# Kernel optimization log

Hardware: AMD Instinct MI355X
Metric: run time of the kernel (lower is better)

Reference implementation:

```python
import jax, jax.numpy as jnp
import numpy as np

B, L, D, H = 4, 1024, 1024, 16
HD = D // H          # head dim = 64
NUM_CASES = 8        # Sanskrit vibhakti cases
SCALE = float(np.sqrt(HD))


def setup_inputs() -> dict:
    key = jax.random.key(0)
    ks = jax.random.split(key, 13)
    s = 0.02
    return {
        "x": jax.random.normal(ks[0], (B, L, D), jnp.float32),
        "case_ids": jax.random.randint(ks[1], (B, L), 0, NUM_CASES, jnp.int32),
        "verb_mask": jax.random.randint(ks[2], (B, L), 0, 2, jnp.int32),
        "Wq": jax.random.normal(ks[3], (D, D), jnp.float32) * s,
        "bq": jnp.zeros((D,), jnp.float32),
        "Wk": jax.random.normal(ks[4], (D, D), jnp.float32) * s,
        "bk": jnp.zeros((D,), jnp.float32),
        "Wv": jax.random.normal(ks[5], (D, D), jnp.float32) * s,
        "bv": jnp.zeros((D,), jnp.float32),
        "Wo": jax.random.normal(ks[6], (D, D), jnp.float32) * s,
        "bo": jnp.zeros((D,), jnp.float32),
        "case_bias": jax.random.normal(ks[7], (H, NUM_CASES, NUM_CASES), jnp.float32) * s,
        "verb_bias": jax.random.normal(ks[8], (H,), jnp.float32) * s,
    }


def reference(x, case_ids, verb_mask, Wq, bq, Wk, bk, Wv, bv, Wo, bo, case_bias, verb_bias):
    b, l, d = x.shape

    def split_heads(t):  # [B,L,D] -> [B,H,L,HD]
        return t.reshape(b, l, H, HD).transpose(0, 2, 1, 3)

    Q = split_heads(x @ Wq + bq)
    K = split_heads(x @ Wk + bk)
    V = split_heads(x @ Wv + bv)

    scores = jnp.einsum('bhid,bhjd->bhij', Q, K) / SCALE  # [B,H,L,L]

    # Panini constraint bias: per-head case-pair bias + per-head verb-position bias
    cb = case_bias[:, case_ids[:, :, None], case_ids[:, None, :]]  # [H,B,L,L]
    cb = cb.transpose(1, 0, 2, 3)                                  # [B,H,L,L]
    vb = verb_bias[None, :, None, None] * verb_mask[:, None, None, :].astype(scores.dtype)
    scores = scores + cb + vb

    weights = jax.nn.softmax(scores, axis=-1)  # dropout is identity in eval
    out = jnp.einsum('bhij,bhjd->bhid', weights, V)       # [B,H,L,HD]
    out = out.transpose(0, 2, 1, 3).reshape(b, l, d)
    return out @ Wo + bo
```

## Files before the change

kernel.cpp:

```cpp
#include <hip/hip_runtime.h>

#define BB 4
#define LL 1024
#define DD 1024
#define HH 16
#define HDD 64

typedef __bf16 bf16x8 __attribute__((ext_vector_type(8)));
typedef float f32x4 __attribute__((ext_vector_type(4)));
typedef float f32x16 __attribute__((ext_vector_type(16)));
typedef unsigned short u16x8 __attribute__((ext_vector_type(8)));
typedef unsigned short u16x4 __attribute__((ext_vector_type(4)));
typedef unsigned int u32x4v __attribute__((ext_vector_type(4)));
typedef unsigned int u32x2 __attribute__((ext_vector_type(2)));

#define LOG2E 1.4426950408889634f

__device__ __forceinline__ unsigned short f2bf(float f) {
    unsigned int u = __builtin_bit_cast(unsigned int, f);
    u += 0x7FFFu + ((u >> 16) & 1u);
    return (unsigned short)(u >> 16);
}

__device__ __forceinline__ unsigned int cvtpk_bf16(float lo, float hi) {
    unsigned int r;
    asm("v_cvt_pk_bf16_f32 %0, %1, %2" : "=v"(r) : "v"(lo), "v"(hi));
    return r;
}

__global__ __launch_bounds__(256) void cvt_x(const float* __restrict__ x,
                                             unsigned short* __restrict__ xb) {
    const int i = (blockIdx.x * 256 + threadIdx.x) * 8;
    f32x4 a0 = *(const f32x4*)(x + i);
    f32x4 a1 = *(const f32x4*)(x + i + 4);
    u16x8 o;
#pragma unroll
    for (int j = 0; j < 4; ++j) { o[j] = f2bf(a0[j]); o[4 + j] = f2bf(a1[j]); }
    *(u16x8*)(xb + i) = o;
}

__global__ __launch_bounds__(256) void trans_w(const float* __restrict__ Wq,
                                               const float* __restrict__ Wk,
                                               const float* __restrict__ Wv,
                                               const float* __restrict__ Wo,
                                               unsigned short* __restrict__ Wqkv_t,
                                               unsigned short* __restrict__ Wo_t) {
    __shared__ unsigned short lds[64 * 72];
    const int t = threadIdx.x;
    const int mat = blockIdx.z;
    const float* W = (mat == 0) ? Wq : (mat == 1) ? Wk : (mat == 2) ? Wv : Wo;
    unsigned short* out = (mat < 3) ? (Wqkv_t + (size_t)mat * 1024 * 1024) : Wo_t;
    const int k0 = blockIdx.x * 64;
    const int n0 = blockIdx.y * 64;
#pragma unroll
    for (int p = 0; p < 4; ++p) {
        int c = t + p * 256;
        int kr = c >> 4, c4 = (c & 15) * 4;
        f32x4 v = *(const f32x4*)(W + (size_t)(k0 + kr) * 1024 + n0 + c4);
#pragma unroll
        for (int i = 0; i < 4; ++i) lds[(c4 + i) * 72 + kr] = f2bf(v[i]);
    }
    __syncthreads();
#pragma unroll
    for (int p = 0; p < 2; ++p) {
        int c = t + p * 256;
        int nr = c >> 3, koff = (c & 7) * 8;
        u16x8 vv = *(const u16x8*)&lds[nr * 72 + koff];
        *(u16x8*)(out + (size_t)(n0 + nr) * 1024 + k0 + koff) = vv;
    }
}

__global__ __launch_bounds__(256) void gemm_qkv(const unsigned short* __restrict__ Abf,
                                                const unsigned short* __restrict__ Btw,
                                                const float* __restrict__ bq,
                                                const float* __restrict__ bk,
                                                const float* __restrict__ bv,
                                                unsigned short* __restrict__ qkv) {
    __shared__ unsigned short Asm[128 * 32];
    __shared__ unsigned short Bsm[128 * 32];
    const int t = threadIdx.x;
    const int w = t >> 6, lane = t & 63;
    const int wm = w >> 1, wn = w & 1;
    const int lr = lane & 15, lk = (lane >> 4) * 8;
    const int row0 = blockIdx.x * 128;
    const int col0 = blockIdx.y * 128;
    const int r = t >> 2;
    const int cb8 = (t & 3) * 8;

    f32x4 acc[4][4];
#pragma unroll
    for (int mf = 0; mf < 4; ++mf)
#pragma unroll
        for (int nf = 0; nf < 4; ++nf)
#pragma unroll
            for (int e = 0; e < 4; ++e) acc[mf][nf][e] = 0.f;

    for (int kt = 0; kt < 32; ++kt) {
        __syncthreads();
        const int k0 = kt * 32;
#pragma unroll
        for (int p = 0; p < 2; ++p) {
            const unsigned short* sa = Abf + (size_t)(row0 + p * 64 + r) * 1024 + k0 + cb8;
            __builtin_amdgcn_global_load_lds(
                (const __attribute__((address_space(1))) unsigned int*)sa,
                (__attribute__((address_space(3))) unsigned int*)(Asm + p * 2048 + t * 8), 16, 0, 0);
            const unsigned short* sb = Btw + (size_t)(col0 + p * 64 + r) * 1024 + k0 + cb8;
            __builtin_amdgcn_global_load_lds(
                (const __attribute__((address_space(1))) unsigned int*)sb,
                (__attribute__((address_space(3))) unsigned int*)(Bsm + p * 2048 + t * 8), 16, 0, 0);
        }
        __syncthreads();
        bf16x8 af[4], bfr[4];
#pragma unroll
        for (int mf = 0; mf < 4; ++mf)
            af[mf] = *(const bf16x8*)&Asm[(wm * 64 + mf * 16 + lr) * 32 + lk];
#pragma unroll
        for (int nf = 0; nf < 4; ++nf)
            bfr[nf] = *(const bf16x8*)&Bsm[(wn * 64 + nf * 16 + lr) * 32 + lk];
#pragma unroll
        for (int mf = 0; mf < 4; ++mf)
#pragma unroll
            for (int nf = 0; nf < 4; ++nf)
                acc[mf][nf] = __builtin_amdgcn_mfma_f32_16x16x32_bf16(af[mf], bfr[nf], acc[mf][nf], 0, 0, 0);
    }

#pragma unroll
    for (int mf = 0; mf < 4; ++mf) {
        const int grow = row0 + wm * 64 + mf * 16 + (lane >> 4) * 4;
#pragma unroll
        for (int nf = 0; nf < 4; ++nf) {
            const int gcol = col0 + wn * 64 + nf * 16 + lr;
            const int mat = gcol >> 10;
            const int nc_ = gcol & 1023;
            const float bias = (mat == 0) ? bq[nc_] : (mat == 1 ? bk[nc_] : bv[nc_]);
            const float scale = (mat == 0) ? 0.125f * LOG2E : 1.0f;
            const int hh = nc_ >> 6, hd = nc_ & 63;
#pragma unroll
            for (int rr = 0; rr < 4; ++rr) {
                const int row = grow + rr;
                const int bb = row >> 10, ll = row & 1023;
                const float vout = (acc[mf][nf][rr] + bias) * scale;
                qkv[((((size_t)mat * BB + bb) * HH + hh) * LL + ll) * HDD + hd] = f2bf(vout);
            }
        }
    }
}

__global__ __launch_bounds__(256) void vtrans(const unsigned short* __restrict__ Vg,
                                              unsigned short* __restrict__ Vt) {
    __shared__ unsigned short lds[64 * 72];
    const int t = threadIdx.x;
    const int bh = blockIdx.y;
    const int j0 = blockIdx.x * 64;
    const size_t hoff = (size_t)bh * LL * HDD;
#pragma unroll
    for (int p = 0; p < 2; ++p) {
        int c = t + p * 256;
        int jr = c >> 3, doff = (c & 7) * 8;
        u16x8 v = *(const u16x8*)(Vg + hoff + (size_t)(j0 + jr) * 64 + doff);
#pragma unroll
        for (int i = 0; i < 8; ++i) lds[(doff + i) * 72 + jr] = v[i];
    }
    __syncthreads();
#pragma unroll
    for (int p = 0; p < 2; ++p) {
        int c = t + p * 256;
        int dr = c >> 3, joff = (c & 7) * 8;
        u16x8 vv = *(const u16x8*)&lds[dr * 72 + joff];
        *(u16x8*)(Vt + hoff + (size_t)dr * 1024 + j0 + joff) = vv;
    }
}

__global__ __launch_bounds__(256) void attn2(const unsigned short* __restrict__ Qg,
                                             const unsigned short* __restrict__ Kg,
                                             const unsigned short* __restrict__ Vtg,
                                             const int* __restrict__ cid,
                                             const int* __restrict__ vmask,
                                             const float* __restrict__ case_bias,
                                             const float* __restrict__ verb_bias,
                                             unsigned short* __restrict__ att) {
    __shared__ unsigned short kvbuf[2][8192];
    __shared__ float tbl[2][8][68];

    const int t = threadIdx.x;
    const int w = t >> 6;
    const int lane = t & 63;
    const int q31 = lane & 31;
    const int g = lane >> 5;

    const int f = blockIdx.x;
    const int qt = (f >> 3) & 7;
    const int bh = ((f & 7) << 3) | (f >> 6);
    const int b = bh >> 4, h = bh & 15;
    const size_t headoff = (size_t)bh * LL * HDD;
    const int q0 = qt * 128;
    const int qrow = q0 + w * 32 + q31;

    bf16x8 qf[4];
    {
        const unsigned short* qp = Qg + headoff + (size_t)qrow * HDD + g * 8;
        qf[0] = *(const bf16x8*)(qp);
        qf[1] = *(const bf16x8*)(qp + 16);
        qf[2] = *(const bf16x8*)(qp + 32);
        qf[3] = *(const bf16x8*)(qp + 48);
    }
    const int cirow = cid[b * LL + qrow] * 68;
    const float vbh = verb_bias[h] * LOG2E;

    float m_run = -1e30f, l_run = 0.f;
    f32x16 acc0, acc1;
#pragma unroll
    for (int e = 0; e < 16; ++e) { acc0[e] = 0.f; acc1[e] = 0.f; }

    const int r8 = lane >> 3, c8 = lane & 7;

#define STAGE(bufn, j0)                                                                            \
    {                                                                                              \
        _Pragma("unroll") for (int cc = 0; cc < 2; ++cc) {                                         \
            const int chunk = w + cc * 4;                                                          \
            const int row = chunk * 8 + r8;                                                        \
            const int sc8 = (c8 ^ (row & 7)) * 8;                                                  \
            const unsigned short* srck = Kg + headoff + (size_t)((j0) + row) * HDD + sc8;          \
            __builtin_amdgcn_global_load_lds(                                                      \
                (const __attribute__((address_space(1))) unsigned int*)srck,                       \
                (__attribute__((address_space(3))) unsigned int*)(&kvbuf[bufn][chunk * 512]), 16,  \
                0, 0);                                                                             \
            const unsigned short* srcv = Vtg + headoff + (size_t)row * LL + (j0) + sc8;            \
            __builtin_amdgcn_global_load_lds(                                                      \
                (const __attribute__((address_space(1))) unsigned int*)srcv,                       \
                (__attribute__((address_space(3))) unsigned int*)(&kvbuf[bufn][4096 + chunk * 512]),\
                16, 0, 0);                                                                         \
        }                                                                                          \
        const int jj = t & 63, ci0 = t >> 6;                                                       \
        const int cj = cid[b * LL + (j0) + jj];                                                    \
        const float vb = vmask[b * LL + (j0) + jj] ? vbh : 0.f;                                    \
        tbl[bufn][ci0][jj] = case_bias[h * 64 + ci0 * 8 + cj] * LOG2E + vb;                        \
        tbl[bufn][ci0 + 4][jj] = case_bias[h * 64 + (ci0 + 4) * 8 + cj] * LOG2E + vb;              \
    }

    STAGE(0, 0);
    __syncthreads();

    for (int jt = 0; jt < 16; ++jt) {
        const int buf = jt & 1;
        if (jt < 15) STAGE(buf ^ 1, (jt + 1) * 64);

        const float* tb = &tbl[buf][0][0] + cirow + 4 * g;
        f32x16 st[2];
#pragma unroll
        for (int jt2 = 0; jt2 < 2; ++jt2) {
            f32x16 s;
#pragma unroll
            for (int r = 0; r < 16; ++r) s[r] = tb[jt2 * 32 + (r & 3) + 8 * (r >> 2)];
            const int arow = jt2 * 32 + q31;
            const unsigned short* kb = &kvbuf[buf][arow * 64];
            const int swz = arow & 7;
#pragma unroll
            for (int kk = 0; kk < 4; ++kk) {
                bf16x8 af = *(const bf16x8*)&kb[((2 * kk + g) ^ swz) * 8];
                s = __builtin_amdgcn_mfma_f32_32x32x16_bf16(af, qf[kk], s, 0, 0, 0);
            }
            st[jt2] = s;
        }

        float mx[16];
#pragma unroll
        for (int r = 0; r < 16; ++r) mx[r] = fmaxf(st[0][r], st[1][r]);
#pragma unroll
        for (int d = 8; d >= 1; d >>= 1)
#pragma unroll
            for (int r = 0; r < 8; ++r)
                if (r < d) mx[r] = fmaxf(mx[r], mx[r + d]);
        float tmax = fmaxf(mx[0], __shfl_xor(mx[0], 32));

        if (!__all(tmax <= m_run + 8.f)) {
            const float mnew = fmaxf(m_run, tmax);
            const float sc = __builtin_amdgcn_exp2f(m_run - mnew);
            m_run = mnew;
            l_run *= sc;
#pragma unroll
            for (int e = 0; e < 16; ++e) { acc0[e] *= sc; acc1[e] *= sc; }
        }

        float tsum = 0.f;
#pragma unroll
        for (int jt2 = 0; jt2 < 2; ++jt2)
#pragma unroll
            for (int r = 0; r < 16; ++r) {
                const float p = __builtin_amdgcn_exp2f(st[jt2][r] - m_run);
                st[jt2][r] = p;
                tsum += p;
            }
        tsum += __shfl_xor(tsum, 32);
        l_run += tsum;

#pragma unroll
        for (int kk = 0; kk < 4; ++kk) {
            const int jt2 = kk >> 1, rb = (kk & 1) * 8;
            unsigned int a0 = cvtpk_bf16(st[jt2][rb + 0], st[jt2][rb + 1]);
            unsigned int b0 = cvtpk_bf16(st[jt2][rb + 4], st[jt2][rb + 5]);
            unsigned int a1 = cvtpk_bf16(st[jt2][rb + 2], st[jt2][rb + 3]);
            unsigned int b1 = cvtpk_bf16(st[jt2][rb + 6], st[jt2][rb + 7]);
            u32x2 r0 = __builtin_amdgcn_permlane32_swap(a0, b0, false, false);
            u32x2 r1 = __builtin_amdgcn_permlane32_swap(a1, b1, false, false);
            u32x4v pw;
            pw[0] = r0[0]; pw[1] = r1[0]; pw[2] = r0[1]; pw[3] = r1[1];
            const bf16x8 pf = __builtin_bit_cast(bf16x8, pw);
#pragma unroll
            for (int dt = 0; dt < 2; ++dt) {
                const int vrow = dt * 32 + q31;
                const bf16x8 vf =
                    *(const bf16x8*)&kvbuf[buf][4096 + vrow * 64 + (((2 * kk + g) ^ (vrow & 7)) * 8)];
                if (dt == 0)
                    acc0 = __builtin_amdgcn_mfma_f32_32x32x16_bf16(vf, pf, acc0, 0, 0, 0);
                else
                    acc1 = __builtin_amdgcn_mfma_f32_32x32x16_bf16(vf, pf, acc1, 0, 0, 0);
            }
        }
        __syncthreads();
    }

    const float inv = 1.0f / l_run;
    unsigned short* ob = &kvbuf[0][0];
    const int orow = w * 32 + q31;
    const int oswz = (orow & 7) << 3;
#pragma unroll
    for (int dt = 0; dt < 2; ++dt) {
#pragma unroll
        for (int u = 0; u < 4; ++u) {
            u16x4 v4;
#pragma unroll
            for (int v = 0; v < 4; ++v)
                v4[v] = f2bf((dt ? acc1[4 * u + v] : acc0[4 * u + v]) * inv);
            const int d0 = dt * 32 + 8 * u + 4 * g;
            *(u16x4*)&ob[orow * 64 + (d0 ^ oswz)] = v4;
        }
    }
    __syncthreads();
#pragma unroll
    for (int p = 0; p < 4; ++p) {
        const int row = p * 32 + (t >> 3);
        const int c16 = t & 7;
        u16x8 v = *(const u16x8*)&ob[row * 64 + ((c16 ^ (row & 7)) * 8)];
        *(u16x8*)(att + (size_t)(b * LL + q0 + row) * DD + h * 64 + c16 * 8) = v;
    }
#undef STAGE
}

__global__ __launch_bounds__(256) void gemm_out(const unsigned short* __restrict__ Abf,
                                                const unsigned short* __restrict__ Btw,
                                                const float* __restrict__ bo,
                                                float* __restrict__ out) {
    __shared__ unsigned short Asm[128 * 32];
    __shared__ unsigned short Bsm[128 * 32];
    const int t = threadIdx.x;
    const int w = t >> 6, lane = t & 63;
    const int wm = w >> 1, wn = w & 1;
    const int lr = lane & 15, lk = (lane >> 4) * 8;
    const int row0 = blockIdx.x * 128;
    const int col0 = blockIdx.y * 128;
    const int r = t >> 2;
    const int cb8 = (t & 3) * 8;

    f32x4 acc[4][4];
#pragma unroll
    for (int mf = 0; mf < 4; ++mf)
#pragma unroll
        for (int nf = 0; nf < 4; ++nf)
#pragma unroll
            for (int e = 0; e < 4; ++e) acc[mf][nf][e] = 0.f;

    for (int kt = 0; kt < 32; ++kt) {
        __syncthreads();
        const int k0 = kt * 32;
#pragma unroll
        for (int p = 0; p < 2; ++p) {
            const unsigned short* sa = Abf + (size_t)(row0 + p * 64 + r) * 1024 + k0 + cb8;
            __builtin_amdgcn_global_load_lds(
                (const __attribute__((address_space(1))) unsigned int*)sa,
                (__attribute__((address_space(3))) unsigned int*)(Asm + p * 2048 + t * 8), 16, 0, 0);
            const unsigned short* sb = Btw + (size_t)(col0 + p * 64 + r) * 1024 + k0 + cb8;
            __builtin_amdgcn_global_load_lds(
                (const __attribute__((address_space(1))) unsigned int*)sb,
                (__attribute__((address_space(3))) unsigned int*)(Bsm + p * 2048 + t * 8), 16, 0, 0);
        }
        __syncthreads();
        bf16x8 af[4], bfr[4];
#pragma unroll
        for (int mf = 0; mf < 4; ++mf)
            af[mf] = *(const bf16x8*)&Asm[(wm * 64 + mf * 16 + lr) * 32 + lk];
#pragma unroll
        for (int nf = 0; nf < 4; ++nf)
            bfr[nf] = *(const bf16x8*)&Bsm[(wn * 64 + nf * 16 + lr) * 32 + lk];
#pragma unroll
        for (int mf = 0; mf < 4; ++mf)
#pragma unroll
            for (int nf = 0; nf < 4; ++nf)
                acc[mf][nf] = __builtin_amdgcn_mfma_f32_16x16x32_bf16(af[mf], bfr[nf], acc[mf][nf], 0, 0, 0);
    }

#pragma unroll
    for (int mf = 0; mf < 4; ++mf) {
        const int grow = row0 + wm * 64 + mf * 16 + (lane >> 4) * 4;
#pragma unroll
        for (int nf = 0; nf < 4; ++nf) {
            const int gcol = col0 + wn * 64 + nf * 16 + lr;
            const float bias = bo[gcol];
#pragma unroll
            for (int rr = 0; rr < 4; ++rr)
                out[(size_t)(grow + rr) * 1024 + gcol] = acc[mf][nf][rr] + bias;
        }
    }
}

extern "C" void kernel_launch(void* const* d_in, const int* in_sizes, int n_in,
                              void* d_out, int out_size, void* d_ws, size_t ws_size,
                              hipStream_t stream) {
    const float* x = (const float*)d_in[0];
    const int* cid = (const int*)d_in[1];
    const int* vmask = (const int*)d_in[2];
    const float* Wq = (const float*)d_in[3];
    const float* bq = (const float*)d_in[4];
    const float* Wk = (const float*)d_in[5];
    const float* bk = (const float*)d_in[6];
    const float* Wv = (const float*)d_in[7];
    const float* bv = (const float*)d_in[8];
    const float* Wo = (const float*)d_in[9];
    const float* bo = (const float*)d_in[10];
    const float* case_bias = (const float*)d_in[11];
    const float* verb_bias = (const float*)d_in[12];
    float* out = (float*)d_out;

    char* ws = (char*)d_ws;
    unsigned short* xb     = (unsigned short*)(ws);
    unsigned short* Wqkv_t = (unsigned short*)(ws + ((size_t)8 << 20));
    unsigned short* Wo_t   = (unsigned short*)(ws + ((size_t)14 << 20));
    unsigned short* qkv    = (unsigned short*)(ws + ((size_t)16 << 20));
    unsigned short* Vt     = (unsigned short*)(ws + ((size_t)40 << 20));
    unsigned short* att    = (unsigned short*)(ws + ((size_t)48 << 20));

    const size_t MATSZ = (size_t)BB * HH * LL * HDD;

    hipLaunchKernelGGL(cvt_x, dim3(2048), dim3(256), 0, stream, x, xb);
    hipLaunchKernelGGL(trans_w, dim3(16, 16, 4), dim3(256), 0, stream, Wq, Wk, Wv, Wo, Wqkv_t, Wo_t);
    hipLaunchKernelGGL(gemm_qkv, dim3(32, 24), dim3(256), 0, stream, xb, Wqkv_t, bq, bk, bv, qkv);
    hipLaunchKernelGGL(vtrans, dim3(16, 64), dim3(256), 0, stream, qkv + 2 * MATSZ, Vt);
    hipLaunchKernelGGL(attn2, dim3(512), dim3(256), 0, stream,
                       qkv, qkv + MATSZ, Vt, cid, vmask, case_bias, verb_bias, att);
    hipLaunchKernelGGL(gemm_out, dim3(32, 8), dim3(256), 0, stream, att, Wo_t, bo, out);
}
```

Measured before the change: 108.5 us.

## Load K/V directly from global in attention, precompute bias table in separate kernel

The attention kernel no longer double-buffers K and V tiles in LDS with barriers. Each wave now reads its MFMA operands straight from global/L2 memory, and the per-iteration __syncthreads is removed. The case/verb bias table is precomputed once per (batch, head) by a new bias_prep kernel and read from global as vectors. s_setprio hints are also added around the MFMA sections. This trades LDS reuse across the 4 waves for redundant global/L2 traffic, since each wave fetches the same K/V independently, and it adds an extra kernel launch.

```diff
diff --git a/kernel.cpp b/kernel.cpp
--- a/kernel.cpp
+++ b/kernel.cpp
@@ -67,6 +67,26 @@
         int nr = c >> 3, koff = (c & 7) * 8;
         u16x8 vv = *(const u16x8*)&lds[nr * 72 + koff];
         *(u16x8*)(out + (size_t)(n0 + nr) * 1024 + k0 + koff) = vv;
+    }
+}
+
+__global__ __launch_bounds__(256) void bias_prep(const int* __restrict__ cid,
+                                                 const int* __restrict__ vmask,
+                                                 const float* __restrict__ case_bias,
+                                                 const float* __restrict__ verb_bias,
+                                                 float* __restrict__ btab) {
+    const int bh = blockIdx.x;
+    const int b = bh >> 4, h = bh & 15;
+    const float vbh = verb_bias[h] * LOG2E;
+    const int t = threadIdx.x;
+#pragma unroll
+    for (int p = 0; p < 4; ++p) {
+        const int j = t + p * 256;
+        const int cj = cid[b * LL + j];
+        const float vb = vmask[b * LL + j] ? vbh : 0.f;
+#pragma unroll
+        for (int ci = 0; ci < 8; ++ci)
+            btab[((size_t)bh * 8 + ci) * LL + j] = case_bias[h * 64 + ci * 8 + cj] * LOG2E + vb;
     }
 }
 
@@ -171,16 +191,13 @@
     }
 }
 
-__global__ __launch_bounds__(256) void attn2(const unsigned short* __restrict__ Qg,
+__global__ __launch_bounds__(256) void attn3(const unsigned short* __restrict__ Qg,
                                              const unsigned short* __restrict__ Kg,
                                              const unsigned short* __restrict__ Vtg,
                                              const int* __restrict__ cid,
-                                             const int* __restrict__ vmask,
-                                             const float* __restrict__ case_bias,
-                                             const float* __restrict__ verb_bias,
+                                             const float* __restrict__ btab,
                                              unsigned short* __restrict__ att) {
-    __shared__ unsigned short kvbuf[2][8192];
-    __shared__ float tbl[2][8][68];
+    __shared__ unsigned short ob[128 * 64];
 
     const int t = threadIdx.x;
     const int w = t >> 6;
@@ -204,62 +221,38 @@
         qf[2] = *(const bf16x8*)(qp + 32);
         qf[3] = *(const bf16x8*)(qp + 48);
     }
-    const int cirow = cid[b * LL + qrow] * 68;
-    const float vbh = verb_bias[h] * LOG2E;
+    const int ci = cid[b * LL + qrow];
+    const float* bias_base = btab + ((size_t)bh * 8 + ci) * LL + 4 * g;
 
     float m_run = -1e30f, l_run = 0.f;
     f32x16 acc0, acc1;
 #pragma unroll
     for (int e = 0; e < 16; ++e) { acc0[e] = 0.f; acc1[e] = 0.f; }
 
-    const int r8 = lane >> 3, c8 = lane & 7;
-
-#define STAGE(bufn, j0)                                                                            \
-    {                                                                                              \
-        _Pragma("unroll") for (int cc = 0; cc < 2; ++cc) {                                         \
-            const int chunk = w + cc * 4;                                                          \
-            const int row = chunk * 8 + r8;                                                        \
-            const int sc8 = (c8 ^ (row & 7)) * 8;                                                  \
-            const unsigned short* srck = Kg + headoff + (size_t)((j0) + row) * HDD + sc8;          \
-            __builtin_amdgcn_global_load_lds(                                                      \
-                (const __attribute__((address_space(1))) unsigned int*)srck,                       \
-                (__attribute__((address_space(3))) unsigned int*)(&kvbuf[bufn][chunk * 512]), 16,  \
-                0, 0);                                                                             \
-            const unsigned short* srcv = Vtg + headoff + (size_t)row * LL + (j0) + sc8;            \
-            __builtin_amdgcn_global_load_lds(                                                      \
-                (const __attribute__((address_space(1))) unsigned int*)srcv,                       \
-                (__attribute__((address_space(3))) unsigned int*)(&kvbuf[bufn][4096 + chunk * 512]),\
-                16, 0, 0);                                                                         \
-        }                                                                                          \
-        const int jj = t & 63, ci0 = t >> 6;                                                       \
-        const int cj = cid[b * LL + (j0) + jj];                                                    \
-        const float vb = vmask[b * LL + (j0) + jj] ? vbh : 0.f;                                    \
-        tbl[bufn][ci0][jj] = case_bias[h * 64 + ci0 * 8 + cj] * LOG2E + vb;                        \
-        tbl[bufn][ci0 + 4][jj] = case_bias[h * 64 + (ci0 + 4) * 8 + cj] * LOG2E + vb;              \
-    }
-
-    STAGE(0, 0);
-    __syncthreads();
+    const unsigned short* kbase = Kg + headoff + (size_t)q31 * HDD + 8 * g;
+    const unsigned short* vbase = Vtg + headoff + (size_t)q31 * LL + 8 * g;
 
     for (int jt = 0; jt < 16; ++jt) {
-        const int buf = jt & 1;
-        if (jt < 15) STAGE(buf ^ 1, (jt + 1) * 64);
-
-        const float* tb = &tbl[buf][0][0] + cirow + 4 * g;
+        const int j0 = jt * 64;
+
+        f32x4 bl[8];
+#pragma unroll
+        for (int c = 0; c < 8; ++c) bl[c] = *(const f32x4*)(bias_base + j0 + 8 * c);
+
         f32x16 st[2];
 #pragma unroll
         for (int jt2 = 0; jt2 < 2; ++jt2) {
             f32x16 s;
 #pragma unroll
-            for (int r = 0; r < 16; ++r) s[r] = tb[jt2 * 32 + (r & 3) + 8 * (r >> 2)];
-            const int arow = jt2 * 32 + q31;
-            const unsigned short* kb = &kvbuf[buf][arow * 64];
-            const int swz = arow & 7;
+            for (int r = 0; r < 16; ++r) s[r] = bl[(r >> 2) + 4 * jt2][r & 3];
+            const unsigned short* kb = kbase + (size_t)(j0 + jt2 * 32) * HDD;
+            __builtin_amdgcn_s_setprio(1);
 #pragma unroll
             for (int kk = 0; kk < 4; ++kk) {
-                bf16x8 af = *(const bf16x8*)&kb[((2 * kk + g) ^ swz) * 8];
+                bf16x8 af = *(const bf16x8*)(kb + 16 * kk);
                 s = __builtin_amdgcn_mfma_f32_32x32x16_bf16(af, qf[kk], s, 0, 0, 0);
             }
+            __builtin_amdgcn_s_setprio(0);
             st[jt2] = s;
         }
 
@@ -294,6 +287,7 @@
         tsum += __shfl_xor(tsum, 32);
         l_run += tsum;
 
+        __builtin_amdgcn_s_setprio(1);
 #pragma unroll
         for (int kk = 0; kk < 4; ++kk) {
             const int jt2 = kk >> 1, rb = (kk & 1) * 8;
@@ -308,20 +302,17 @@
             const bf16x8 pf = __builtin_bit_cast(bf16x8, pw);
 #pragma unroll
             for (int dt = 0; dt < 2; ++dt) {
-                const int vrow = dt * 32 + q31;
-                const bf16x8 vf =
-                    *(const bf16x8*)&kvbuf[buf][4096 + vrow * 64 + (((2 * kk + g) ^ (vrow & 7)) * 8)];
+                const bf16x8 vf = *(const bf16x8*)(vbase + (size_t)(dt * 32) * LL + j0 + 16 * kk);
                 if (dt == 0)
                     acc0 = __builtin_amdgcn_mfma_f32_32x32x16_bf16(vf, pf, acc0, 0, 0, 0);
                 else
                     acc1 = __builtin_amdgcn_mfma_f32_32x32x16_bf16(vf, pf, acc1, 0, 0, 0);
             }
         }
-        __syncthreads();
+        __builtin_amdgcn_s_setprio(0);
     }
 
     const float inv = 1.0f / l_run;
-    unsigned short* ob = &kvbuf[0][0];
     const int orow = w * 32 + q31;
     const int oswz = (orow & 7) << 3;
 #pragma unroll
@@ -344,7 +335,6 @@
         u16x8 v = *(const u16x8*)&ob[row * 64 + ((c16 ^ (row & 7)) * 8)];
         *(u16x8*)(att + (size_t)(b * LL + q0 + row) * DD + h * 64 + c16 * 8) = v;
     }
-#undef STAGE
 }
 
 __global__ __launch_bounds__(256) void gemm_out(const unsigned short* __restrict__ Abf,
@@ -438,14 +428,16 @@
     unsigned short* qkv    = (unsigned short*)(ws + ((size_t)16 << 20));
     unsigned short* Vt     = (unsigned short*)(ws + ((size_t)40 << 20));
     unsigned short* att    = (unsigned short*)(ws + ((size_t)48 << 20));
+    float*          btab   = (float*)(ws + ((size_t)56 << 20));
 
     const size_t MATSZ = (size_t)BB * HH * LL * HDD;
 
     hipLaunchKernelGGL(cvt_x, dim3(2048), dim3(256), 0, stream, x, xb);
     hipLaunchKernelGGL(trans_w, dim3(16, 16, 4), dim3(256), 0, stream, Wq, Wk, Wv, Wo, Wqkv_t, Wo_t);
+    hipLaunchKernelGGL(bias_prep, dim3(64), dim3(256), 0, stream, cid, vmask, case_bias, verb_bias, btab);
     hipLaunchKernelGGL(gemm_qkv, dim3(32, 24), dim3(256), 0, stream, xb, Wqkv_t, bq, bk, bv, qkv);
     hipLaunchKernelGGL(vtrans, dim3(16, 64), dim3(256), 0, stream, qkv + 2 * MATSZ, Vt);
-    hipLaunchKernelGGL(attn2, dim3(512), dim3(256), 0, stream,
-                       qkv, qkv + MATSZ, Vt, cid, vmask, case_bias, verb_bias, att);
+    hipLaunchKernelGGL(attn3, dim3(512), dim3(256), 0, stream,
+                       qkv, qkv + MATSZ, Vt, cid, btab, att);
     hipLaunchKernelGGL(gemm_out, dim3(32, 8), dim3(256), 0, stream, att, Wo_t, bo, out);
 }
```

Result: slower. 161.0 us (+48.4%).

## Precompute bias table, halve attention tile, explicit double-buffer with prefetched bias registers

Applied to the files above, without the earlier changes.

A new prep kernel builds a per-(batch, head, query-case) table of the combined case and verb bias, laid out in MFMA accumulator order. The attention kernel then loads its bias straight into registers instead of rebuilding an LDS table on every key tile. The attention kernel moves to 128 threads handling 64 query rows, with 1024 blocks and launch bounds of two blocks per unit. The key-tile loop is unrolled by two with explicit waitcnt and barrier handling, and s_setprio is raised around the MFMA sections. In exchange it adds a launch, a small extra global table, and K/V reloads across twice as many blocks.

```diff
diff --git a/kernel.cpp b/kernel.cpp
--- a/kernel.cpp
+++ b/kernel.cpp
@@ -67,6 +67,26 @@
         int nr = c >> 3, koff = (c & 7) * 8;
         u16x8 vv = *(const u16x8*)&lds[nr * 72 + koff];
         *(u16x8*)(out + (size_t)(n0 + nr) * 1024 + k0 + koff) = vv;
+    }
+}
+
+__global__ __launch_bounds__(256) void bias_prep3(const int* __restrict__ cid,
+                                                  const int* __restrict__ vmask,
+                                                  const float* __restrict__ case_bias,
+                                                  const float* __restrict__ verb_bias,
+                                                  float* __restrict__ btab3) {
+    const int bh = blockIdx.x;
+    const int b = bh >> 4, h = bh & 15;
+    const float vbh = verb_bias[h] * LOG2E;
+    for (int idx = threadIdx.x; idx < 8192; idx += 256) {
+        const int ci = idx >> 10;
+        const int g = (idx >> 9) & 1;
+        const int pos = idx & 511;
+        const int jt = pos >> 5, jt2 = (pos >> 4) & 1, r = pos & 15;
+        const int j = jt * 64 + jt2 * 32 + (r & 3) + 8 * (r >> 2) + 4 * g;
+        const int cj = cid[b * LL + j];
+        const float vb = vmask[b * LL + j] ? vbh : 0.f;
+        btab3[(size_t)bh * 8192 + idx] = case_bias[h * 64 + ci * 8 + cj] * LOG2E + vb;
     }
 }
 
@@ -171,30 +191,107 @@
     }
 }
 
-__global__ __launch_bounds__(256) void attn2(const unsigned short* __restrict__ Qg,
-                                             const unsigned short* __restrict__ Kg,
-                                             const unsigned short* __restrict__ Vtg,
-                                             const int* __restrict__ cid,
-                                             const int* __restrict__ vmask,
-                                             const float* __restrict__ case_bias,
-                                             const float* __restrict__ verb_bias,
-                                             unsigned short* __restrict__ att) {
+__device__ __forceinline__ void ctile64(const unsigned short* kvb, const f32x4 (&bb)[8],
+                                        const bf16x8 (&qf)[4], int q31, int g,
+                                        f32x16& acc0, f32x16& acc1, float& m_run, float& l_run) {
+    f32x16 st[2];
+#pragma unroll
+    for (int jt2 = 0; jt2 < 2; ++jt2) {
+        f32x16 s;
+#pragma unroll
+        for (int r = 0; r < 16; ++r) s[r] = bb[jt2 * 4 + (r >> 2)][r & 3];
+        const int arow = jt2 * 32 + q31;
+        const unsigned short* kb = &kvb[arow * 64];
+        const int swz = arow & 7;
+        __builtin_amdgcn_s_setprio(1);
+#pragma unroll
+        for (int kk = 0; kk < 4; ++kk) {
+            const bf16x8 af = *(const bf16x8*)&kb[((2 * kk + g) ^ swz) * 8];
+            s = __builtin_amdgcn_mfma_f32_32x32x16_bf16(af, qf[kk], s, 0, 0, 0);
+        }
+        __builtin_amdgcn_s_setprio(0);
+        st[jt2] = s;
+    }
+
+    float mx[16];
+#pragma unroll
+    for (int r = 0; r < 16; ++r) mx[r] = fmaxf(st[0][r], st[1][r]);
+#pragma unroll
+    for (int d = 8; d >= 1; d >>= 1)
+#pragma unroll
+        for (int r = 0; r < 8; ++r)
+            if (r < d) mx[r] = fmaxf(mx[r], mx[r + d]);
+    float tmax = fmaxf(mx[0], __shfl_xor(mx[0], 32));
+
+    if (!__all(tmax <= m_run + 8.f)) {
+        const float mnew = fmaxf(m_run, tmax);
+        const float sc = __builtin_amdgcn_exp2f(m_run - mnew);
+        m_run = mnew;
+        l_run *= sc;
+#pragma unroll
+        for (int e = 0; e < 16; ++e) { acc0[e] *= sc; acc1[e] *= sc; }
+    }
+
+    float tsum = 0.f;
+#pragma unroll
+    for (int jt2 = 0; jt2 < 2; ++jt2)
+#pragma unroll
+        for (int r = 0; r < 16; ++r) {
+            const float p = __builtin_amdgcn_exp2f(st[jt2][r] - m_run);
+            st[jt2][r] = p;
+            tsum += p;
+        }
+    tsum += __shfl_xor(tsum, 32);
+    l_run += tsum;
+
+    __builtin_amdgcn_s_setprio(1);
+#pragma unroll
+    for (int kk = 0; kk < 4; ++kk) {
+        const int jt2 = kk >> 1, rb = (kk & 1) * 8;
+        unsigned int a0 = cvtpk_bf16(st[jt2][rb + 0], st[jt2][rb + 1]);
+        unsigned int b0 = cvtpk_bf16(st[jt2][rb + 4], st[jt2][rb + 5]);
+        unsigned int a1 = cvtpk_bf16(st[jt2][rb + 2], st[jt2][rb + 3]);
+        unsigned int b1 = cvtpk_bf16(st[jt2][rb + 6], st[jt2][rb + 7]);
+        u32x2 r0 = __builtin_amdgcn_permlane32_swap(a0, b0, false, false);
+        u32x2 r1 = __builtin_amdgcn_permlane32_swap(a1, b1, false, false);
+        u32x4v pw;
+        pw[0] = r0[0]; pw[1] = r1[0]; pw[2] = r0[1]; pw[3] = r1[1];
+        const bf16x8 pf = __builtin_bit_cast(bf16x8, pw);
+#pragma unroll
+        for (int dt = 0; dt < 2; ++dt) {
+            const int vrow = dt * 32 + q31;
+            const bf16x8 vf =
+                *(const bf16x8*)&kvb[4096 + vrow * 64 + (((2 * kk + g) ^ (vrow & 7)) * 8)];
+            if (dt == 0)
+                acc0 = __builtin_amdgcn_mfma_f32_32x32x16_bf16(vf, pf, acc0, 0, 0, 0);
+            else
+                acc1 = __builtin_amdgcn_mfma_f32_32x32x16_bf16(vf, pf, acc1, 0, 0, 0);
+        }
+    }
+    __builtin_amdgcn_s_setprio(0);
+}
+
+__global__ __launch_bounds__(128, 2) void attn7(const unsigned short* __restrict__ Qg,
+                                                const unsigned short* __restrict__ Kg,
+                                                const unsigned short* __restrict__ Vtg,
+                                                const int* __restrict__ cid,
+                                                const float* __restrict__ btab3,
+                                                unsigned short* __restrict__ att) {
     __shared__ unsigned short kvbuf[2][8192];
-    __shared__ float tbl[2][8][68];
 
     const int t = threadIdx.x;
-    const int w = t >> 6;
+    const int w2 = t >> 6;
     const int lane = t & 63;
     const int q31 = lane & 31;
     const int g = lane >> 5;
 
     const int f = blockIdx.x;
-    const int qt = (f >> 3) & 7;
-    const int bh = ((f & 7) << 3) | (f >> 6);
+    const int qt = (f >> 3) & 15;
+    const int bh = ((f & 7) << 3) | (f >> 7);
     const int b = bh >> 4, h = bh & 15;
     const size_t headoff = (size_t)bh * LL * HDD;
-    const int q0 = qt * 128;
-    const int qrow = q0 + w * 32 + q31;
+    const int q0 = qt * 64;
+    const int qrow = q0 + w2 * 32 + q31;
 
     bf16x8 qf[4];
     {
@@ -204,125 +301,65 @@
         qf[2] = *(const bf16x8*)(qp + 32);
         qf[3] = *(const bf16x8*)(qp + 48);
     }
-    const int cirow = cid[b * LL + qrow] * 68;
-    const float vbh = verb_bias[h] * LOG2E;
-
-    float m_run = -1e30f, l_run = 0.f;
-    f32x16 acc0, acc1;
-#pragma unroll
-    for (int e = 0; e < 16; ++e) { acc0[e] = 0.f; acc1[e] = 0.f; }
+    const int ci = cid[b * LL + qrow];
+    const float* bbase = btab3 + ((size_t)(bh * 8 + ci) * 2 + g) * 512;
 
     const int r8 = lane >> 3, c8 = lane & 7;
 
-#define STAGE(bufn, j0)                                                                            \
+#define STAGE(bufn, j0s)                                                                           \
     {                                                                                              \
-        _Pragma("unroll") for (int cc = 0; cc < 2; ++cc) {                                         \
-            const int chunk = w + cc * 4;                                                          \
+        _Pragma("unroll") for (int cc = 0; cc < 4; ++cc) {                                         \
+            const int chunk = w2 + cc * 2;                                                         \
             const int row = chunk * 8 + r8;                                                        \
             const int sc8 = (c8 ^ (row & 7)) * 8;                                                  \
-            const unsigned short* srck = Kg + headoff + (size_t)((j0) + row) * HDD + sc8;          \
+            const unsigned short* srck = Kg + headoff + (size_t)((j0s) + row) * HDD + sc8;         \
             __builtin_amdgcn_global_load_lds(                                                      \
                 (const __attribute__((address_space(1))) unsigned int*)srck,                       \
                 (__attribute__((address_space(3))) unsigned int*)(&kvbuf[bufn][chunk * 512]), 16,  \
                 0, 0);                                                                             \
-            const unsigned short* srcv = Vtg + headoff + (size_t)row * LL + (j0) + sc8;            \
+            const unsigned short* srcv = Vtg + headoff + (size_t)row * LL + (j0s) + sc8;           \
             __builtin_amdgcn_global_load_lds(                                                      \
                 (const __attribute__((address_space(1))) unsigned int*)srcv,                       \
                 (__attribute__((address_space(3))) unsigned int*)(&kvbuf[bufn][4096 + chunk * 512]),\
                 16, 0, 0);                                                                         \
         }                                                                                          \
-        const int jj = t & 63, ci0 = t >> 6;                                                       \
-        const int cj = cid[b * LL + (j0) + jj];                                                    \
-        const float vb = vmask[b * LL + (j0) + jj] ? vbh : 0.f;                                    \
-        tbl[bufn][ci0][jj] = case_bias[h * 64 + ci0 * 8 + cj] * LOG2E + vb;                        \
-        tbl[bufn][ci0 + 4][jj] = case_bias[h * 64 + (ci0 + 4) * 8 + cj] * LOG2E + vb;              \
-    }
-
+    }
+
+    float m_run = -1e30f, l_run = 0.f;
+    f32x16 acc0, acc1;
+#pragma unroll
+    for (int e = 0; e < 16; ++e) { acc0[e] = 0.f; acc1[e] = 0.f; }
+
+    f32x4 bA[8], bB[8];
     STAGE(0, 0);
+#pragma unroll
+    for (int i = 0; i < 8; ++i) bA[i] = *(const f32x4*)(bbase + 4 * i);
+
+    for (int jt = 0; jt < 16; jt += 2) {
+        asm volatile("s_waitcnt vmcnt(0)" ::: "memory");
+        __builtin_amdgcn_s_barrier();
+        asm volatile("" ::: "memory");
+        STAGE(1, (jt + 1) * 64);
+#pragma unroll
+        for (int i = 0; i < 8; ++i) bB[i] = *(const f32x4*)(bbase + (jt + 1) * 32 + 4 * i);
+        ctile64(&kvbuf[0][0], bA, qf, q31, g, acc0, acc1, m_run, l_run);
+
+        asm volatile("s_waitcnt vmcnt(0)" ::: "memory");
+        __builtin_amdgcn_s_barrier();
+        asm volatile("" ::: "memory");
+        if (jt + 2 < 16) {
+            STAGE(0, (jt + 2) * 64);
+#pragma unroll
+            for (int i = 0; i < 8; ++i) bA[i] = *(const f32x4*)(bbase + (jt + 2) * 32 + 4 * i);
+        }
+        ctile64(&kvbuf[1][0], bB, qf, q31, g, acc0, acc1, m_run, l_run);
+    }
+#undef STAGE
+
     __syncthreads();
-
-    for (int jt = 0; jt < 16; ++jt) {
-        const int buf = jt & 1;
-        if (jt < 15) STAGE(buf ^ 1, (jt + 1) * 64);
-
-        const float* tb = &tbl[buf][0][0] + cirow + 4 * g;
-        f32x16 st[2];
-#pragma unroll
-        for (int jt2 = 0; jt2 < 2; ++jt2) {
-            f32x16 s;
-#pragma unroll
-            for (int r = 0; r < 16; ++r) s[r] = tb[jt2 * 32 + (r & 3) + 8 * (r >> 2)];
-            const int arow = jt2 * 32 + q31;
-            const unsigned short* kb = &kvbuf[buf][arow * 64];
-            const int swz = arow & 7;
-#pragma unroll
-            for (int kk = 0; kk < 4; ++kk) {
-                bf16x8 af = *(const bf16x8*)&kb[((2 * kk + g) ^ swz) * 8];
-                s = __builtin_amdgcn_mfma_f32_32x32x16_bf16(af, qf[kk], s, 0, 0, 0);
-            }
-            st[jt2] = s;
-        }
-
-        float mx[16];
-#pragma unroll
-        for (int r = 0; r < 16; ++r) mx[r] = fmaxf(st[0][r], st[1][r]);
-#pragma unroll
-        for (int d = 8; d >= 1; d >>= 1)
-#pragma unroll
-            for (int r = 0; r < 8; ++r)
-                if (r < d) mx[r] = fmaxf(mx[r], mx[r + d]);
-        float tmax = fmaxf(mx[0], __shfl_xor(mx[0], 32));
-
-        if (!__all(tmax <= m_run + 8.f)) {
-            const float mnew = fmaxf(m_run, tmax);
-            const float sc = __builtin_amdgcn_exp2f(m_run - mnew);
-            m_run = mnew;
-            l_run *= sc;
-#pragma unroll
-            for (int e = 0; e < 16; ++e) { acc0[e] *= sc; acc1[e] *= sc; }
-        }
-
-        float tsum = 0.f;
-#pragma unroll
-        for (int jt2 = 0; jt2 < 2; ++jt2)
-#pragma unroll
-            for (int r = 0; r < 16; ++r) {
-                const float p = __builtin_amdgcn_exp2f(st[jt2][r] - m_run);
-                st[jt2][r] = p;
-                tsum += p;
-            }
-        tsum += __shfl_xor(tsum, 32);
-        l_run += tsum;
-
-#pragma unroll
-        for (int kk = 0; kk < 4; ++kk) {
-            const int jt2 = kk >> 1, rb = (kk & 1) * 8;
-            unsigned int a0 = cvtpk_bf16(st[jt2][rb + 0], st[jt2][rb + 1]);
-            unsigned int b0 = cvtpk_bf16(st[jt2][rb + 4], st[jt2][rb + 5]);
-            unsigned int a1 = cvtpk_bf16(st[jt2][rb + 2], st[jt2][rb + 3]);
-            unsigned int b1 = cvtpk_bf16(st[jt2][rb + 6], st[jt2][rb + 7]);
-            u32x2 r0 = __builtin_amdgcn_permlane32_swap(a0, b0, false, false);
-            u32x2 r1 = __builtin_amdgcn_permlane32_swap(a1, b1, false, false);
-            u32x4v pw;
-            pw[0] = r0[0]; pw[1] = r1[0]; pw[2] = r0[1]; pw[3] = r1[1];
-            const bf16x8 pf = __builtin_bit_cast(bf16x8, pw);
-#pragma unroll
-            for (int dt = 0; dt < 2; ++dt) {
-                const int vrow = dt * 32 + q31;
-                const bf16x8 vf =
-                    *(const bf16x8*)&kvbuf[buf][4096 + vrow * 64 + (((2 * kk + g) ^ (vrow & 7)) * 8)];
-                if (dt == 0)
-                    acc0 = __builtin_amdgcn_mfma_f32_32x32x16_bf16(vf, pf, acc0, 0, 0, 0);
-                else
-                    acc1 = __builtin_amdgcn_mfma_f32_32x32x16_bf16(vf, pf, acc1, 0, 0, 0);
-            }
-        }
-        __syncthreads();
-    }
-
     const float inv = 1.0f / l_run;
     unsigned short* ob = &kvbuf[0][0];
-    const int orow = w * 32 + q31;
+    const int orow = w2 * 32 + q31;
     const int oswz = (orow & 7) << 3;
 #pragma unroll
     for (int dt = 0; dt < 2; ++dt) {
@@ -339,12 +376,12 @@
     __syncthreads();
 #pragma unroll
     for (int p = 0; p < 4; ++p) {
-        const int row = p * 32 + (t >> 3);
-        const int c16 = t & 7;
+        const int sl = p * 128 + t;
+        const int row = sl >> 3;
+        const int c16 = sl & 7;
         u16x8 v = *(const u16x8*)&ob[row * 64 + ((c16 ^ (row & 7)) * 8)];
         *(u16x8*)(att + (size_t)(b * LL + q0 + row) * DD + h * 64 + c16 * 8) = v;
     }
-#undef STAGE
 }
 
 __global__ __launch_bounds__(256) void gemm_out(const unsigned short* __restrict__ Abf,
@@ -438,14 +475,16 @@
     unsigned short* qkv    = (unsigned short*)(ws + ((size_t)16 << 20));
     unsigned short* Vt     = (unsigned short*)(ws + ((size_t)40 << 20));
     unsigned short* att    = (unsigned short*)(ws + ((size_t)48 << 20));
+    float*          btab3  = (float*)(ws + ((size_t)56 << 20));
 
     const size_t MATSZ = (size_t)BB * HH * LL * HDD;
 
     hipLaunchKernelGGL(cvt_x, dim3(2048), dim3(256), 0, stream, x, xb);
     hipLaunchKernelGGL(trans_w, dim3(16, 16, 4), dim3(256), 0, stream, Wq, Wk, Wv, Wo, Wqkv_t, Wo_t);
+    hipLaunchKernelGGL(bias_prep3, dim3(64), dim3(256), 0, stream, cid, vmask, case_bias, verb_bias, btab3);
     hipLaunchKernelGGL(gemm_qkv, dim3(32, 24), dim3(256), 0, stream, xb, Wqkv_t, bq, bk, bv, qkv);
     hipLaunchKernelGGL(vtrans, dim3(16, 64), dim3(256), 0, stream, qkv + 2 * MATSZ, Vt);
-    hipLaunchKernelGGL(attn2, dim3(512), dim3(256), 0, stream,
-                       qkv, qkv + MATSZ, Vt, cid, vmask, case_bias, verb_bias, att);
+    hipLaunchKernelGGL(attn7, dim3(1024), dim3(128), 0, stream,
+                       qkv, qkv + MATSZ, Vt, cid, btab3, att);
     hipLaunchKernelGGL(gemm_out, dim3(32, 8), dim3(256), 0, stream, att, Wo_t, bo, out);
 }
```

After: 119.9 us. 10.5% more time.
